# Kernel optimization log

Hardware: AMD Instinct MI355X
Metric: run time of the kernel (lower is better)

Reference implementation:

```python
import jax, jax.numpy as jnp
import numpy as np

N_NODE, N_EDGE = 8192, 4096
D_NODE, D_EDGE, D_GLOBAL = 64, 16, 8


def _dense(key, fan_in, fan_out):
    kw, kb = jax.random.split(key)
    W = jax.random.normal(kw, (fan_in, fan_out), dtype=jnp.float32) * 0.02
    b = jnp.zeros((fan_out,), dtype=jnp.float32)
    return W, b


def setup_inputs() -> dict:
    key = jax.random.key(0)
    ks = jax.random.split(key, 16)
    nodes = jax.random.normal(ks[0], (N_NODE, D_NODE), dtype=jnp.float32)
    edges = jax.random.normal(ks[1], (N_EDGE, D_EDGE), dtype=jnp.float32)
    globals_ = jax.random.normal(ks[2], (1, D_GLOBAL), dtype=jnp.float32)
    senders = jax.random.randint(ks[3], (N_EDGE,), 0, N_NODE, dtype=jnp.int32)
    receivers = jax.random.randint(ks[4], (N_EDGE,), 0, N_NODE, dtype=jnp.int32)
    # edge MLP: input = concat(edges, nodes[s], nodes[r], globals); widths [N_EDGE]*2
    e_in = D_EDGE + 2 * D_NODE + D_GLOBAL
    eW1, eb1 = _dense(ks[5], e_in, N_EDGE)
    eW2, eb2 = _dense(ks[6], N_EDGE, N_EDGE)
    # node MLP: input = concat(nodes, sent_agg, recv_agg, globals); widths [D_NODE]*2
    n_in = D_NODE + 2 * N_EDGE + D_GLOBAL
    nW1, nb1 = _dense(ks[7], n_in, D_NODE)
    nW2, nb2 = _dense(ks[8], D_NODE, D_NODE)
    return {"nodes": nodes, "edges": edges, "globals_": globals_,
            "senders": senders, "receivers": receivers,
            "eW1": eW1, "eb1": eb1, "eW2": eW2, "eb2": eb2,
            "nW1": nW1, "nb1": nb1, "nW2": nW2, "nb2": nb2}


def reference(nodes, edges, globals_, senders, receivers,
              eW1, eb1, eW2, eb2, nW1, nb1, nW2, nb2):
    n_node, n_edge = nodes.shape[0], edges.shape[0]
    g = globals_[0]  # single graph: broadcast its global feature row
    # --- edge update: concat(edges, sent node feats, received node feats, globals) ---
    g_e = jnp.broadcast_to(g, (n_edge, g.shape[0]))
    e_in = jnp.concatenate([edges, nodes[senders], nodes[receivers], g_e], axis=-1)
    h = jax.nn.relu(e_in @ eW1 + eb1)          # [E, E]
    new_edges = jax.nn.relu(h @ eW2 + eb2)     # [E, E]
    # --- aggregate edges to nodes (jraph default: segment_sum by senders and receivers) ---
    sent_agg = jax.ops.segment_sum(new_edges, senders, num_segments=n_node)
    recv_agg = jax.ops.segment_sum(new_edges, receivers, num_segments=n_node)
    # --- node update: concat(nodes, sent_agg, recv_agg, globals) ---
    g_n = jnp.broadcast_to(g, (n_node, g.shape[0]))
    n_in = jnp.concatenate([nodes, sent_agg, recv_agg, g_n], axis=-1)
    h2 = jax.nn.relu(n_in @ nW1 + nb1)         # [N, D_NODE]
    new_nodes = jax.nn.relu(h2 @ nW2 + nb2)    # [N, D_NODE]
    # globals unchanged (update_global_fn=None)
    return new_nodes, new_edges
```

## Files before the change

### kernel.cpp

```cpp
#include <hip/hip_runtime.h>

typedef unsigned short u16;
typedef unsigned int u32;
typedef unsigned long long u64;
typedef __bf16 bf16x8 __attribute__((ext_vector_type(8)));
typedef float f32x4 __attribute__((ext_vector_type(4)));

static __device__ __forceinline__ float bf2f(u16 u) {
  return __uint_as_float(((u32)u) << 16);
}
static __device__ __forceinline__ u16 f2bf(float f) {
  u32 x = __float_as_uint(f);
  return (u16)((x + 0x7fffu + ((x >> 16) & 1u)) >> 16);
}
static __device__ __forceinline__ void gl_lds16(const u16* g, u16* l) {
  __builtin_amdgcn_global_load_lds(
      (const __attribute__((address_space(1))) void*)g,
      (__attribute__((address_space(3))) void*)l, 16, 0, 0);
}
static __device__ __forceinline__ u64 pack4bf(f32x4 v) {
  u64 r = (u64)f2bf(v[0]);
  r |= (u64)f2bf(v[1]) << 16;
  r |= (u64)f2bf(v[2]) << 32;
  r |= (u64)f2bf(v[3]) << 48;
  return r;
}

__global__ __launch_bounds__(256) void k_transpose(const float* __restrict__ in,
                                                   u16* __restrict__ out,
                                                   int K, int N, int Kpad) {
  __shared__ u16 t[64 * 68];
  const int tid = threadIdx.x;
  const int k0 = blockIdx.x * 64, n0 = blockIdx.y * 64;
#pragma unroll
  for (int pass = 0; pass < 4; pass++) {
    int ki = pass * 16 + (tid >> 4);
    int nj = (tid & 15) * 4;
    f32x4 v = {0.f, 0.f, 0.f, 0.f};
    if (k0 + ki < K) v = *(const f32x4*)&in[(long)(k0 + ki) * N + n0 + nj];
    *(u64*)&t[ki * 68 + nj] = pack4bf(v);
  }
  __syncthreads();
#pragma unroll
  for (int pass = 0; pass < 4; pass++) {
    int ni = pass * 16 + (tid >> 4);
    int kj = (tid & 15) * 4;
    if (k0 + kj < Kpad) {
      u64 w = (u64)t[(kj + 0) * 68 + ni] | ((u64)t[(kj + 1) * 68 + ni] << 16) |
              ((u64)t[(kj + 2) * 68 + ni] << 32) | ((u64)t[(kj + 3) * 68 + ni] << 48);
      *(u64*)&out[(long)(n0 + ni) * Kpad + k0 + kj] = w;
    }
  }
}

__global__ __launch_bounds__(192) void k_build_ein(const float* __restrict__ edges,
                                                   const float* __restrict__ nodes,
                                                   const float* __restrict__ g,
                                                   const int* __restrict__ senders,
                                                   const int* __restrict__ receivers,
                                                   u16* __restrict__ ein) {
  const int e = blockIdx.x;
  const int x = threadIdx.x;
  if (x >= 160) return;
  const int s = senders[e], r = receivers[e];
  float v;
  if (x < 16) v = edges[(long)e * 16 + x];
  else if (x < 80) v = nodes[(long)s * 64 + (x - 16)];
  else if (x < 144) v = nodes[(long)r * 64 + (x - 80)];
  else if (x < 152) v = g[x - 144];
  else v = 0.f;
  ein[(long)e * 160 + x] = f2bf(v);
}

template <int MODE>
__global__ __launch_bounds__(256) void k_mgemm(const u16* __restrict__ A,
                                               const u16* __restrict__ BT,
                                               const float* __restrict__ bias,
                                               void* __restrict__ C, int M, int N, int K) {
  __shared__ alignas(16) u16 As[128 * 32];
  __shared__ alignas(16) u16 Bs[128 * 32];
  const int tid = threadIdx.x;
  const int lane = tid & 63, wid = tid >> 6;
  const int wr = wid >> 1, wc = wid & 1;
  const int m0 = blockIdx.x * 128, n0 = blockIdx.y * 128;
  const int lr = lane & 15, lk = lane >> 4;
  const int swz = (lk ^ ((lr >> 1) & 3)) << 3;
  const int srow = tid >> 2;
  const int skk = ((tid & 3) ^ ((tid >> 3) & 3)) << 3;

  f32x4 acc[4][4];
#pragma unroll
  for (int i = 0; i < 4; i++)
#pragma unroll
    for (int j = 0; j < 4; j++) acc[i][j] = {0.f, 0.f, 0.f, 0.f};

  for (int kt = 0; kt < K; kt += 32) {
#pragma unroll
    for (int rep = 0; rep < 2; rep++) {
      int row = rep * 64 + srow;
      int o = rep * 2048 + tid * 8;
      gl_lds16(&A[(long)(m0 + row) * K + kt + skk], &As[o]);
      gl_lds16(&BT[(long)(n0 + row) * K + kt + skk], &Bs[o]);
    }
    __syncthreads();
    bf16x8 af[4], bfr[4];
#pragma unroll
    for (int mi = 0; mi < 4; mi++)
      af[mi] = *(const bf16x8*)&As[(wr * 64 + mi * 16 + lr) * 32 + swz];
#pragma unroll
    for (int ni = 0; ni < 4; ni++)
      bfr[ni] = *(const bf16x8*)&Bs[(wc * 64 + ni * 16 + lr) * 32 + swz];
#pragma unroll
    for (int mi = 0; mi < 4; mi++)
#pragma unroll
      for (int ni = 0; ni < 4; ni++)
        acc[mi][ni] =
            __builtin_amdgcn_mfma_f32_16x16x32_bf16(af[mi], bfr[ni], acc[mi][ni], 0, 0, 0);
    __syncthreads();
  }
#pragma unroll
  for (int ni = 0; ni < 4; ni++) {
    int col = n0 + wc * 64 + ni * 16 + lr;
    float bb = bias[col];
#pragma unroll
    for (int mi = 0; mi < 4; mi++) {
      int row = m0 + wr * 64 + mi * 16 + lk * 4;
#pragma unroll
      for (int r = 0; r < 4; r++) {
        float v = fmaxf(acc[mi][ni][r] + bb, 0.f);
        if (MODE == 0) ((u16*)C)[(long)(row + r) * N + col] = f2bf(v);
        else ((float*)C)[(long)(row + r) * N + col] = v;
      }
    }
  }
}

__global__ __launch_bounds__(512, 1) void k_gemm256(const u16* __restrict__ A,
                                                    const u16* __restrict__ BT,
                                                    const float* __restrict__ bias,
                                                    float* __restrict__ C, int N, int K) {
  __shared__ alignas(16) u16 lds[65536];
  const int tid = threadIdx.x;
  const int lane = tid & 63, wid = tid >> 6;
  const int wr = wid >> 2, wc = wid & 3;
  const int orig = blockIdx.x;
  const int xc = orig & 7, jj = orig >> 3;
  const int m0 = (2 * xc + (jj >> 4)) * 256;
  const int n0 = (jj & 15) * 256;
  const int lr = lane & 15, lk = lane >> 4;
  const int NT = K >> 6;

  const int sgran = ((tid & 7) ^ ((tid >> 3) & 7)) << 3;
  const int sdst = tid * 8;
  const long abase = (long)(m0 + (tid >> 3)) * K + sgran;
  const long bbase = (long)(n0 + (tid >> 3)) * K + sgran;

  f32x4 acc[8][4];
#pragma unroll
  for (int i = 0; i < 8; i++)
#pragma unroll
    for (int j = 0; j < 4; j++) acc[i][j] = {0.f, 0.f, 0.f, 0.f};

#define STAGE64(T, BUF)                                     \
  {                                                         \
    const long ko_ = (long)(T) * 64;                        \
    u16* Ab_ = &lds[(BUF) * 32768];                         \
    u16* Bb_ = Ab_ + 16384;                                 \
    gl_lds16(&A[abase + ko_], Ab_ + sdst);                  \
    gl_lds16(&A[abase + (long)64 * K + ko_], Ab_ + 4096 + sdst);   \
    gl_lds16(&A[abase + (long)128 * K + ko_], Ab_ + 8192 + sdst);  \
    gl_lds16(&A[abase + (long)192 * K + ko_], Ab_ + 12288 + sdst); \
    gl_lds16(&BT[bbase + ko_], Bb_ + sdst);                 \
    gl_lds16(&BT[bbase + (long)64 * K + ko_], Bb_ + 4096 + sdst);  \
    gl_lds16(&BT[bbase + (long)128 * K + ko_], Bb_ + 8192 + sdst); \
    gl_lds16(&BT[bbase + (long)192 * K + ko_], Bb_ + 12288 + sdst);\
  }

#define RSWZ(R, G) (((R) * 64) + ((((G) ^ ((R) & 7))) << 3))

#define PHASE(KS, AbP, BbP)                                                        \
  {                                                                                \
    bf16x8 af[8], bfr[4];                                                          \
    _Pragma("unroll") for (int mi = 0; mi < 8; mi++)                               \
        af[mi] = *(const bf16x8*)&AbP[RSWZ(wr * 128 + mi * 16 + lr, lk + 4 * (KS))]; \
    _Pragma("unroll") for (int ni = 0; ni < 4; ni++)                               \
        bfr[ni] = *(const bf16x8*)&BbP[RSWZ(wc * 64 + ni * 16 + lr, lk + 4 * (KS))]; \
    asm volatile("s_waitcnt lgkmcnt(0)" ::: "memory");                             \
    __builtin_amdgcn_sched_barrier(0);                                             \
    __builtin_amdgcn_s_setprio(1);                                                 \
    _Pragma("unroll") for (int mi = 0; mi < 8; mi++)                               \
        _Pragma("unroll") for (int ni = 0; ni < 4; ni++)                           \
            acc[mi][ni] = __builtin_amdgcn_mfma_f32_16x16x32_bf16(af[mi], bfr[ni], \
                                                                  acc[mi][ni],    \
                                                                  0, 0, 0);        \
    __builtin_amdgcn_s_setprio(0);                                                 \
  }

  STAGE64(0, 0)
  STAGE64(1, 1)

  for (int t = 0; t < NT; t++) {
    if (t == NT - 1) {
      asm volatile("s_waitcnt vmcnt(0)" ::: "memory");
    } else {
      asm volatile("s_waitcnt vmcnt(8)" ::: "memory");
    }
    __builtin_amdgcn_s_barrier();
    const u16* Ab = &lds[(t & 1) * 32768];
    const u16* Bb = Ab + 16384;
    PHASE(0, Ab, Bb)
    PHASE(1, Ab, Bb)
    __builtin_amdgcn_s_barrier();
    if (t + 2 < NT) STAGE64(t + 2, t & 1)
  }
#undef PHASE
#undef RSWZ
#undef STAGE64

#pragma unroll
  for (int ni = 0; ni < 4; ni++) {
    int col = n0 + wc * 64 + ni * 16 + lr;
    float bb = bias[col];
#pragma unroll
    for (int mi = 0; mi < 8; mi++) {
      int row = m0 + wr * 128 + mi * 16 + lk * 4;
#pragma unroll
      for (int r = 0; r < 4; r++)
        C[(long)(row + r) * N + col] = fmaxf(acc[mi][ni][r] + bb, 0.f);
    }
  }
}

__global__ __launch_bounds__(256) void k_scatter_m(const float* __restrict__ E,
                                                   const u16* __restrict__ BT,
                                                   const int* __restrict__ senders,
                                                   const int* __restrict__ receivers,
                                                   float* __restrict__ accb) {
  const int K = 4096;
  __shared__ alignas(16) u16 As[128 * 32];
  __shared__ alignas(16) u16 Bs[128 * 32];
  const int tid = threadIdx.x;
  const int lane = tid & 63, wid = tid >> 6;
  const int wr = wid >> 1, wc = wid & 1;
  const int m0 = blockIdx.x * 128;
  const int kbase = blockIdx.y * 512;
  const int lr = lane & 15, lk = lane >> 4;
  const int swz = (lk ^ ((lr >> 1) & 3)) << 3;
  const int srow = tid >> 2;
  const int skk = ((tid & 3) ^ ((tid >> 3) & 3)) << 3;

  f32x4 acc[4][4];
#pragma unroll
  for (int i = 0; i < 4; i++)
#pragma unroll
    for (int j = 0; j < 4; j++) acc[i][j] = {0.f, 0.f, 0.f, 0.f};

  for (int kt = kbase; kt < kbase + 512; kt += 32) {
#pragma unroll
    for (int p = 0; p < 4; p++) {
      int idx = p * 256 + tid;
      int r = idx >> 3;
      int kq = idx & 7;
      f32x4 v = *(const f32x4*)&E[(long)(m0 + r) * 4096 + kt + kq * 4];
      int gq = (kq >> 1) ^ ((r >> 1) & 3);
      *(u64*)&As[r * 32 + gq * 8 + (kq & 1) * 4] = pack4bf(v);
    }
#pragma unroll
    for (int rep = 0; rep < 2; rep++) {
      int row = rep * 64 + srow;
      gl_lds16(&BT[(long)row * K + kt + skk], &Bs[rep * 2048 + tid * 8]);
    }
    __syncthreads();
    bf16x8 af[4], bfr[4];
#pragma unroll
    for (int mi = 0; mi < 4; mi++)
      af[mi] = *(const bf16x8*)&As[(wr * 64 + mi * 16 + lr) * 32 + swz];
#pragma unroll
    for (int ni = 0; ni < 4; ni++)
      bfr[ni] = *(const bf16x8*)&Bs[(wc * 64 + ni * 16 + lr) * 32 + swz];
#pragma unroll
    for (int mi = 0; mi < 4; mi++)
#pragma unroll
      for (int ni = 0; ni < 4; ni++)
        acc[mi][ni] =
            __builtin_amdgcn_mfma_f32_16x16x32_bf16(af[mi], bfr[ni], acc[mi][ni], 0, 0, 0);
    __syncthreads();
  }
#pragma unroll
  for (int mi = 0; mi < 4; mi++) {
#pragma unroll
    for (int r = 0; r < 4; r++) {
      int e = m0 + wr * 64 + mi * 16 + lk * 4 + r;
#pragma unroll
      for (int ni = 0; ni < 4; ni++) {
        int col = wc * 64 + ni * 16 + lr;
        int tgt = (col < 64) ? senders[e] : receivers[e];
        atomicAdd(&accb[(long)tgt * 64 + (col & 63)], acc[mi][ni][r]);
      }
    }
  }
}

__global__ __launch_bounds__(256) void k_final(const float* __restrict__ nodes,
                                               const float* __restrict__ g,
                                               const float* __restrict__ nW1,
                                               const float* __restrict__ nb1,
                                               const float* __restrict__ nW2,
                                               const float* __restrict__ nb2,
                                               const float* __restrict__ zpre,
                                               float* __restrict__ out0) {
  __shared__ float h2[64 * 64];
  __shared__ float gb[64];
  const int tid = threadIdx.x;
  const long n0 = (long)blockIdx.x * 64;
  if (tid < 64) {
    float s = nb1[tid];
#pragma unroll
    for (int j = 0; j < 8; j++) s += g[j] * nW1[(long)(8256 + j) * 64 + tid];
    gb[tid] = s;
  }
  __syncthreads();
#pragma unroll 2
  for (int rep = 0; rep < 16; rep++) {
    int idx = rep * 256 + tid;
    int i = idx >> 6, c = idx & 63;
    float z = gb[c] + zpre[(n0 + i) * 64 + c];
    const float* nr = nodes + (n0 + i) * 64;
#pragma unroll 8
    for (int k = 0; k < 64; k++) z += nr[k] * nW1[(long)k * 64 + c];
    h2[idx] = fmaxf(z, 0.f);
  }
  __syncthreads();
#pragma unroll 2
  for (int rep = 0; rep < 16; rep++) {
    int idx = rep * 256 + tid;
    int i = idx >> 6, c = idx & 63;
    float z = nb2[c];
#pragma unroll 8
    for (int k = 0; k < 64; k++) z += h2[i * 64 + k] * nW2[(long)k * 64 + c];
    out0[(n0 + i) * 64 + c] = fmaxf(z, 0.f);
  }
}

extern "C" void kernel_launch(void* const* d_in, const int* in_sizes, int n_in,
                              void* d_out, int out_size, void* d_ws, size_t ws_size,
                              hipStream_t stream) {
  const float* nodes = (const float*)d_in[0];
  const float* edges = (const float*)d_in[1];
  const float* g = (const float*)d_in[2];
  const int* senders = (const int*)d_in[3];
  const int* receivers = (const int*)d_in[4];
  const float* eW1 = (const float*)d_in[5];
  const float* eb1 = (const float*)d_in[6];
  const float* eW2 = (const float*)d_in[7];
  const float* eb2 = (const float*)d_in[8];
  const float* nW1 = (const float*)d_in[9];
  const float* nb1 = (const float*)d_in[10];
  const float* nW2 = (const float*)d_in[11];
  const float* nb2 = (const float*)d_in[12];

  char* ws = (char*)d_ws;
  u16* eW1T = (u16*)(ws + 0);
  float* accb = (float*)(ws + 0);
  u16* ein = (u16*)(ws + 2097152);
  u16* nWmT = (u16*)(ws + 2097152);
  u16* eW2T = (u16*)(ws + 3407872);
  u16* h = (u16*)(ws + 36962304);

  float* out_nodes = (float*)d_out;
  float* out_edges = (float*)d_out + 524288;

  dim3 b256(256);
  k_transpose<<<dim3(3, 64), b256, 0, stream>>>(eW1, eW1T, 152, 4096, 160);
  k_transpose<<<dim3(64, 64), b256, 0, stream>>>(eW2, eW2T, 4096, 4096, 4096);
  k_build_ein<<<4096, 192, 0, stream>>>(edges, nodes, g, senders, receivers, ein);

  k_mgemm<0><<<dim3(32, 32), b256, 0, stream>>>(ein, eW1T, eb1, h, 4096, 4096, 160);

  k_transpose<<<dim3(64, 1), b256, 0, stream>>>(nW1 + 64 * 64, nWmT, 4096, 64, 4096);
  k_transpose<<<dim3(64, 1), b256, 0, stream>>>(nW1 + 4160 * 64, nWmT + (long)64 * 4096,
                                                4096, 64, 4096);
  hipMemsetAsync(accb, 0, 8192 * 64 * 4, stream);

  k_gemm256<<<dim3(256), dim3(512), 0, stream>>>(h, eW2T, eb2, out_edges, 4096, 4096);

  k_scatter_m<<<dim3(32, 8), b256, 0, stream>>>(out_edges, nWmT, senders, receivers, accb);
  k_final<<<128, b256, 0, stream>>>(nodes, g, nW1, nb1, nW2, nb2, accb, out_nodes);
}
```

Before: 251.1 us.

## Split GEMM k-step into four half-M phases with barrier-interleaved LDS reads

Restructures the main GEMM inner loop so each 64-wide k-tile is processed in four sub-phases over half of the M fragments, each reading fewer LDS fragments before its MFMA burst, with workgroup barriers around every MFMA block. The vmcnt wait and barrier move to after the next prefetch is issued. The aim is to cut register pressure and let the LDS reads of one wave overlap the MFMAs of others, ping-pong style. In exchange it adds eight barriers per k-tile, which could stall waves if they are not balanced.

```diff
diff --git a/kernel.cpp b/kernel.cpp
--- a/kernel.cpp
+++ b/kernel.cpp
@@ -161,16 +161,16 @@
 #pragma unroll
     for (int j = 0; j < 4; j++) acc[i][j] = {0.f, 0.f, 0.f, 0.f};
 
-#define STAGE64(T, BUF)                                     \
-  {                                                         \
-    const long ko_ = (long)(T) * 64;                        \
-    u16* Ab_ = &lds[(BUF) * 32768];                         \
-    u16* Bb_ = Ab_ + 16384;                                 \
-    gl_lds16(&A[abase + ko_], Ab_ + sdst);                  \
+#define STAGE64(T, BUF)                                            \
+  {                                                                \
+    const long ko_ = (long)(T) * 64;                               \
+    u16* Ab_ = &lds[(BUF) * 32768];                                \
+    u16* Bb_ = Ab_ + 16384;                                        \
+    gl_lds16(&A[abase + ko_], Ab_ + sdst);                         \
     gl_lds16(&A[abase + (long)64 * K + ko_], Ab_ + 4096 + sdst);   \
     gl_lds16(&A[abase + (long)128 * K + ko_], Ab_ + 8192 + sdst);  \
     gl_lds16(&A[abase + (long)192 * K + ko_], Ab_ + 12288 + sdst); \
-    gl_lds16(&BT[bbase + ko_], Bb_ + sdst);                 \
+    gl_lds16(&BT[bbase + ko_], Bb_ + sdst);                        \
     gl_lds16(&BT[bbase + (long)64 * K + ko_], Bb_ + 4096 + sdst);  \
     gl_lds16(&BT[bbase + (long)128 * K + ko_], Bb_ + 8192 + sdst); \
     gl_lds16(&BT[bbase + (long)192 * K + ko_], Bb_ + 12288 + sdst);\
@@ -178,42 +178,59 @@
 
 #define RSWZ(R, G) (((R) * 64) + ((((G) ^ ((R) & 7))) << 3))
 
-#define PHASE(KS, AbP, BbP)                                                        \
-  {                                                                                \
-    bf16x8 af[8], bfr[4];                                                          \
-    _Pragma("unroll") for (int mi = 0; mi < 8; mi++)                               \
-        af[mi] = *(const bf16x8*)&AbP[RSWZ(wr * 128 + mi * 16 + lr, lk + 4 * (KS))]; \
-    _Pragma("unroll") for (int ni = 0; ni < 4; ni++)                               \
-        bfr[ni] = *(const bf16x8*)&BbP[RSWZ(wc * 64 + ni * 16 + lr, lk + 4 * (KS))]; \
-    asm volatile("s_waitcnt lgkmcnt(0)" ::: "memory");                             \
-    __builtin_amdgcn_sched_barrier(0);                                             \
-    __builtin_amdgcn_s_setprio(1);                                                 \
-    _Pragma("unroll") for (int mi = 0; mi < 8; mi++)                               \
-        _Pragma("unroll") for (int ni = 0; ni < 4; ni++)                           \
-            acc[mi][ni] = __builtin_amdgcn_mfma_f32_16x16x32_bf16(af[mi], bfr[ni], \
-                                                                  acc[mi][ni],    \
-                                                                  0, 0, 0);        \
-    __builtin_amdgcn_s_setprio(0);                                                 \
-  }
+#define RD_A(AF, AbP, MH, KS)                                                        \
+  _Pragma("unroll") for (int mi = 0; mi < 4; mi++)                                   \
+      AF[mi] = *(const bf16x8*)&AbP[RSWZ(wr * 128 + (MH) * 64 + mi * 16 + lr,        \
+                                         lk + 4 * (KS))];
+
+#define RD_B(BF, BbP, KS)                                                            \
+  _Pragma("unroll") for (int ni = 0; ni < 4; ni++)                                   \
+      BF[ni] = *(const bf16x8*)&BbP[RSWZ(wc * 64 + ni * 16 + lr, lk + 4 * (KS))];
+
+#define WAIT_MFMA(AF, BF, MH)                                                        \
+  __builtin_amdgcn_s_barrier();                                                      \
+  asm volatile("s_waitcnt lgkmcnt(0)" ::: "memory");                                 \
+  __builtin_amdgcn_sched_barrier(0);                                                 \
+  __builtin_amdgcn_s_setprio(1);                                                     \
+  _Pragma("unroll") for (int mi = 0; mi < 4; mi++)                                   \
+      _Pragma("unroll") for (int ni = 0; ni < 4; ni++)                               \
+          acc[(MH) * 4 + mi][ni] = __builtin_amdgcn_mfma_f32_16x16x32_bf16(          \
+              AF[mi], BF[ni], acc[(MH) * 4 + mi][ni], 0, 0, 0);                      \
+  __builtin_amdgcn_s_setprio(0);                                                     \
+  __builtin_amdgcn_s_barrier();
 
   STAGE64(0, 0)
   STAGE64(1, 1)
+  asm volatile("s_waitcnt vmcnt(8)" ::: "memory");
+  __builtin_amdgcn_s_barrier();
 
   for (int t = 0; t < NT; t++) {
-    if (t == NT - 1) {
-      asm volatile("s_waitcnt vmcnt(0)" ::: "memory");
-    } else {
-      asm volatile("s_waitcnt vmcnt(8)" ::: "memory");
-    }
-    __builtin_amdgcn_s_barrier();
     const u16* Ab = &lds[(t & 1) * 32768];
     const u16* Bb = Ab + 16384;
-    PHASE(0, Ab, Bb)
-    PHASE(1, Ab, Bb)
-    __builtin_amdgcn_s_barrier();
+    bf16x8 afA[4], bfA[4], afB[4], bfB[4];
+    RD_A(afA, Ab, 0, 0)
+    RD_B(bfA, Bb, 0)
+    WAIT_MFMA(afA, bfA, 0)
+    RD_A(afB, Ab, 1, 0)
+    WAIT_MFMA(afB, bfA, 1)
+    RD_A(afA, Ab, 0, 1)
+    RD_B(bfB, Bb, 1)
+    WAIT_MFMA(afA, bfB, 0)
+    RD_A(afB, Ab, 1, 1)
+    WAIT_MFMA(afB, bfB, 1)
     if (t + 2 < NT) STAGE64(t + 2, t & 1)
-  }
-#undef PHASE
+    if (t + 1 < NT) {
+      if (t + 2 < NT) {
+        asm volatile("s_waitcnt vmcnt(8)" ::: "memory");
+      } else {
+        asm volatile("s_waitcnt vmcnt(0)" ::: "memory");
+      }
+      __builtin_amdgcn_s_barrier();
+    }
+  }
+#undef WAIT_MFMA
+#undef RD_B
+#undef RD_A
 #undef RSWZ
 #undef STAGE64
 
```

After: 262.1 us. 4.4% more time.
